# Kernel optimization log

Measured on AMD Instinct MI355X. Metric: run time of the kernel, lower is better.

Reference implementation:

```python
import jax, jax.numpy as jnp
import numpy as np

B, T, P, D = 8, 512, 2048, 768
TOKEN_HALF = 0.15
PATCH_HALF = 0.03  # small patch boxes


def _make_boxes(key, b, n, half):
    c = jax.random.uniform(key, (b, n, 2), dtype=jnp.float32)
    lo = jnp.clip(c - half, 0.0, 1.0)
    hi = jnp.clip(c + half, 0.0, 1.0)
    return jnp.concatenate([lo, hi], axis=-1)  # (b, n, 4): x0,y0,x1,y1


def setup_inputs() -> dict:
    key = jax.random.key(0)
    k1, k2, k3, k4 = jax.random.split(key, 4)
    patch_feats = jax.random.normal(k1, (B, P, D), dtype=jnp.float32)
    token_boxes = _make_boxes(k2, B, T, TOKEN_HALF)
    patch_boxes = _make_boxes(k3, B, P, PATCH_HALF)
    token_mask = jnp.ones((B, T), dtype=bool)
    scorer_w = jax.random.normal(k4, (D,), dtype=jnp.float32) * 0.02
    scorer_b = jnp.zeros((1,), dtype=jnp.float32)
    return {"patch_feats": patch_feats, "token_boxes": token_boxes,
            "patch_boxes": patch_boxes, "token_mask": token_mask,
            "scorer_w": scorer_w, "scorer_b": scorer_b}


def _patches_in_token_boxes(patch_boxes, tb):
    # patch center containment test: (B,T,P) bool
    cx = 0.5 * (patch_boxes[..., 0] + patch_boxes[..., 2])  # (B,P)
    cy = 0.5 * (patch_boxes[..., 1] + patch_boxes[..., 3])  # (B,P)
    cx = cx[:, None, :]
    cy = cy[:, None, :]
    return ((cx >= tb[..., 0:1]) & (cx <= tb[..., 2:3]) &
            (cy >= tb[..., 1:2]) & (cy <= tb[..., 3:4]))


def reference(patch_feats, token_boxes, patch_boxes, token_mask, scorer_w, scorer_b):
    # normalize token boxes if given in 0..1000 coords (data-dependent, via where)
    tb = token_boxes
    scale = jnp.where(tb.max() > 1.5, jnp.float32(1.0 / 1000.0), jnp.float32(1.0))
    tb = tb * scale

    in_box = _patches_in_token_boxes(patch_boxes, tb)          # (B,T,P)
    in_box = in_box & token_mask[:, :, None]
    region_mask = jnp.any(in_box, axis=-1)                      # (B,T)

    scores = patch_feats @ scorer_w + scorer_b[0]               # (B,P)
    scores = jnp.broadcast_to(scores[:, None, :], in_box.shape)  # (B,T,P)
    scores = jnp.where(in_box, scores, jnp.float32(-10000.0))
    attn = jax.nn.softmax(scores, axis=-1)                      # (B,T,P)

    region_feats = jnp.einsum('btp,bpd->btd', attn, patch_feats)
    region_feats = region_feats * region_mask[..., None].astype(region_feats.dtype)
    return region_feats, region_mask
```

## Files before the change

kernel.cpp:

```cpp
#include <hip/hip_runtime.h>

#define B 8
#define T 512
#define P 2048
#define D 768
#define KDIM P
#define NSPLIT 2
#define KSPLIT (KDIM / NSPLIT)

typedef unsigned short ushort_t;
using short8 = __attribute__((ext_vector_type(8))) short;
using f32x4v = __attribute__((ext_vector_type(4))) float;

#define IDX_SCALE 0
#define IDX_SCORES 64
#define IDX_SCORES2 (64 + B*P)
#define IDX_CX (64 + B*P)
#define IDX_CY (64 + 2*B*P)
#define OFF_ATTN_BYTES 197120
#define OFF_FT_BYTES (OFF_ATTN_BYTES + (size_t)B*T*P*2)
#define OFF_PART_BYTES (OFF_FT_BYTES + (size_t)B*D*P*2)
#define WS_NEED (OFF_PART_BYTES + (size_t)NSPLIT*B*T*D*4)

#define GLD16(gsrc, ldst) \
    __builtin_amdgcn_global_load_lds((const __attribute__((address_space(1))) void*)(gsrc), \
                                     (__attribute__((address_space(3))) void*)(ldst), 16, 0, 0)

#define SCHED_FENCE() __builtin_amdgcn_sched_barrier(0)
#define RAW_BARRIER() do { SCHED_FENCE(); __builtin_amdgcn_s_barrier(); SCHED_FENCE(); } while (0)

__device__ inline ushort_t f2bf(float x) {
    union { float f; unsigned u; } v; v.f = x;
    unsigned r = v.u + 0x7fffu + ((v.u >> 16) & 1u);
    return (ushort_t)(r >> 16);
}

__global__ void k_scale(const float* __restrict__ tboxes, float* __restrict__ ws) {
    __shared__ float red[4];
    int tid = threadIdx.x;
    float m = -1e30f;
    const float4* tb4 = (const float4*)tboxes;
    #pragma unroll
    for (int i = 0; i < 16; ++i) {
        float4 v = tb4[tid + i * 256];
        m = fmaxf(fmaxf(fmaxf(m, v.x), fmaxf(v.y, v.z)), v.w);
    }
    #pragma unroll
    for (int off = 1; off < 64; off <<= 1) m = fmaxf(m, __shfl_xor(m, off));
    if ((tid & 63) == 0) red[tid >> 6] = m;
    __syncthreads();
    if (tid == 0) {
        float mb = fmaxf(fmaxf(red[0], red[1]), fmaxf(red[2], red[3]));
        ws[IDX_SCALE] = (mb > 1.5f) ? (1.0f / 1000.0f) : 1.0f;
    }
}

__global__ __launch_bounds__(256) void k_prep(const float* __restrict__ feats,
        const float* __restrict__ w, float* __restrict__ ws, ushort_t* __restrict__ fT) {
    __shared__ float tile[2][64][65];
    __shared__ float sred[64][17];
    const int t = threadIdx.x;
    const int p0 = blockIdx.x * 64;
    const int z = blockIdx.y;
    const int b = blockIdx.z;
    const float4* f4 = (const float4*)(feats + ((size_t)b * P + p0) * D);
    const float4* w4 = (const float4*)w;
    const int tr = t >> 4, tc = t & 15;
    float sp[4] = {0.f, 0.f, 0.f, 0.f};

    float4 v[4];
    {
        int dt = z * 6;
        #pragma unroll
        for (int i = 0; i < 4; ++i)
            v[i] = f4[(size_t)(tr + 16 * i) * 192 + dt * 16 + tc];
    }
    int cur = 0;
    for (int it = 0; it < 6; ++it) {
        const int dt = z * 6 + it;
        float4 wv = w4[dt * 16 + tc];
        #pragma unroll
        for (int i = 0; i < 4; ++i) {
            int pr = tr + 16 * i;
            sp[i] += v[i].x * wv.x + v[i].y * wv.y + v[i].z * wv.z + v[i].w * wv.w;
            tile[cur][pr][tc * 4 + 0] = v[i].x;
            tile[cur][pr][tc * 4 + 1] = v[i].y;
            tile[cur][pr][tc * 4 + 2] = v[i].z;
            tile[cur][pr][tc * 4 + 3] = v[i].w;
        }
        __syncthreads();
        if (it < 5) {
            int dt2 = dt + 1;
            #pragma unroll
            for (int i = 0; i < 4; ++i)
                v[i] = f4[(size_t)(tr + 16 * i) * 192 + dt2 * 16 + tc];
        }
        #pragma unroll
        for (int pass = 0; pass < 4; ++pass) {
            int idx = pass * 256 + t;
            int dr = idx >> 4;
            int pq = (idx & 15) * 4;
            unsigned u0 = (unsigned)f2bf(tile[cur][pq + 0][dr]) |
                          ((unsigned)f2bf(tile[cur][pq + 1][dr]) << 16);
            unsigned u1 = (unsigned)f2bf(tile[cur][pq + 2][dr]) |
                          ((unsigned)f2bf(tile[cur][pq + 3][dr]) << 16);
            uint2 o; o.x = u0; o.y = u1;
            *(uint2*)&fT[((size_t)b * D + dt * 64 + dr) * P + p0 + pq] = o;
        }
        cur ^= 1;
    }
    #pragma unroll
    for (int i = 0; i < 4; ++i) sred[tr + 16 * i][tc] = sp[i];
    __syncthreads();
    if (t < 64) {
        float s = 0.f;
        #pragma unroll
        for (int c = 0; c < 16; ++c) s += sred[t][c];
        ws[(z ? IDX_SCORES2 : IDX_SCORES) + b * P + p0 + t] = s;
    }
}

__global__ __launch_bounds__(256) void k_attn(const float* __restrict__ tboxes,
        const float* __restrict__ pboxes, const unsigned char* __restrict__ mask8,
        const float* __restrict__ bias, const float* __restrict__ ws,
        ushort_t* __restrict__ attn, float* __restrict__ out) {
    const int wv = threadIdx.x >> 6;
    const int ln = threadIdx.x & 63;
    const int t = blockIdx.x * 4 + wv;
    const int b = blockIdx.y;
    const int row = b * T + t;
    const float scale = ws[IDX_SCALE];
    const float bs = bias[0];
    const float4 tb = ((const float4*)tboxes)[row];
    const float lox = tb.x * scale, loy = tb.y * scale;
    const float hix = tb.z * scale, hiy = tb.w * scale;
    bool storage_u8 = ((mask8[1] | mask8[2] | mask8[3]) != 0);
    bool tmask = storage_u8 ? (mask8[row] != 0) : (((const int*)mask8)[row] != 0);

    const float2* sA = (const float2*)(ws + IDX_SCORES + b * P);
    const float2* sB = (const float2*)(ws + IDX_SCORES2 + b * P);
    const float4* pb4 = (const float4*)(pboxes + (size_t)b * P * 4);
    unsigned* arow32 = (unsigned*)(attn + (size_t)row * P);

    float s0[16], s1[16];
    float m = -1e30f;
    const float NINF = -__builtin_inff();
    #pragma unroll
    for (int r = 0; r < 16; ++r) {
        int q = ln + 64 * r;
        float2 sa = sA[q], sb = sB[q];
        float v0 = sa.x + sb.x + bs;
        float v1 = sa.y + sb.y + bs;
        float4 b0 = pb4[2 * q], b1 = pb4[2 * q + 1];
        float cx0 = 0.5f * (b0.x + b0.z), cy0 = 0.5f * (b0.y + b0.w);
        float cx1 = 0.5f * (b1.x + b1.z), cy1 = 0.5f * (b1.y + b1.w);
        bool i0 = (cx0 >= lox) && (cx0 <= hix) && (cy0 >= loy) && (cy0 <= hiy);
        bool i1 = (cx1 >= lox) && (cx1 <= hix) && (cy1 >= loy) && (cy1 <= hiy);
        s0[r] = i0 ? v0 : NINF;
        s1[r] = i1 ? v1 : NINF;
        m = fmaxf(m, fmaxf(s0[r], s1[r]));
    }
    #pragma unroll
    for (int off = 1; off < 64; off <<= 1) m = fmaxf(m, __shfl_xor(m, off));
    bool any = m > -1e29f;

    if (!any || !tmask) {
        #pragma unroll
        for (int r = 0; r < 16; ++r) arow32[ln + 64 * r] = 0u;
        if (ln == 0) out[(size_t)B * T * D + row] = 0.f;
        return;
    }
    float lsum = 0.f;
    #pragma unroll
    for (int r = 0; r < 16; ++r) {
        s0[r] = __expf(s0[r] - m);
        s1[r] = __expf(s1[r] - m);
        lsum += s0[r] + s1[r];
    }
    #pragma unroll
    for (int off = 1; off < 64; off <<= 1) lsum += __shfl_xor(lsum, off);
    float invl = 1.0f / lsum;
    #pragma unroll
    for (int r = 0; r < 16; ++r) {
        unsigned lo = (unsigned)f2bf(s0[r] * invl);
        unsigned hi = (unsigned)f2bf(s1[r] * invl);
        arow32[ln + 64 * r] = lo | (hi << 16);
    }
    if (ln == 0) out[(size_t)B * T * D + row] = 1.0f;
}

__global__ __launch_bounds__(256, 2) void k_gemm(const ushort_t* __restrict__ attn,
        const ushort_t* __restrict__ fT, float* __restrict__ partial) {
    __shared__ __align__(16) ushort_t As[2 * 8192];
    __shared__ __align__(16) ushort_t Bs[2 * 8192];
    const int tid = threadIdx.x;
    const int lane = tid & 63, wid = tid >> 6;
    const int wm = wid >> 1, wn = wid & 1;

    const int bid = blockIdx.x;
    const int b = bid & 7;
    const int rem = bid >> 3;
    const int s = (rem >= 24) ? 1 : 0;
    const int tile = (rem >= 24) ? rem - 24 : rem;
    const int t0 = (tile & 3) * 128;
    const int n0 = (tile >> 2) * 128;
    const int kbase = s * KSPLIT;

    const ushort_t* Ab = attn + ((size_t)b * T + t0) * P + kbase;
    const ushort_t* Bb = fT + ((size_t)b * D + n0) * P + kbase;

    const int rl8 = lane >> 3;
    const int slot = (lane & 7) ^ rl8;

    f32x4v acc[4][4];
    #pragma unroll
    for (int i = 0; i < 4; ++i)
        #pragma unroll
        for (int j = 0; j < 4; ++j)
            acc[i][j] = (f32x4v){0.f, 0.f, 0.f, 0.f};

    const int lr = lane & 15, hi4 = lane >> 4;

    #define STAGE(buf, kt) do { \
        const ushort_t* a_src = Ab + (size_t)(kt) * 64; \
        const ushort_t* b_src = Bb + (size_t)(kt) * 64; \
        _Pragma("unroll") \
        for (int i = 0; i < 4; ++i) { \
            int c = wid * 4 + i; \
            GLD16(a_src + (size_t)(c * 8 + rl8) * P + slot * 8, &As[(buf) * 8192 + c * 512]); \
        } \
        _Pragma("unroll") \
        for (int i = 0; i < 4; ++i) { \
            int c = wid * 4 + i; \
            GLD16(b_src + (size_t)(c * 8 + rl8) * P + slot * 8, &Bs[(buf) * 8192 + c * 512]); \
        } \
    } while (0)

    #define LDA(row, kslot) (((row) >> 3) * 512 + ((row) & 7) * 64 + (((kslot) ^ ((row) & 7)) * 8))

    #define COMPUTE(buf) do { \
        _Pragma("unroll") \
        for (int ks = 0; ks < 2; ++ks) { \
            short8 a[4], bfr[4]; \
            int kslot = ks * 4 + hi4; \
            _Pragma("unroll") \
            for (int i = 0; i < 4; ++i) \
                a[i] = *(const short8*)&As[(buf) * 8192 + LDA(wm * 64 + i * 16 + lr, kslot)]; \
            _Pragma("unroll") \
            for (int j = 0; j < 4; ++j) \
                bfr[j] = *(const short8*)&Bs[(buf) * 8192 + LDA(wn * 64 + j * 16 + lr, kslot)]; \
            _Pragma("unroll") \
            for (int i = 0; i < 4; ++i) \
                _Pragma("unroll") \
                for (int j = 0; j < 4; ++j) \
                    acc[i][j] = __builtin_amdgcn_mfma_f32_16x16x32_bf16(a[i], bfr[j], acc[i][j], 0, 0, 0); \
        } \
    } while (0)

    STAGE(0, 0);
    int cur = 0;
    for (int kt = 0; kt < KSPLIT / 64 - 1; ++kt) {
        STAGE(cur ^ 1, kt + 1);
        asm volatile("s_waitcnt vmcnt(8)" ::: "memory");
        RAW_BARRIER();
        COMPUTE(cur);
        RAW_BARRIER();
        cur ^= 1;
    }
    asm volatile("s_waitcnt vmcnt(0)" ::: "memory");
    RAW_BARRIER();
    COMPUTE(cur);

    float* pout = partial + (size_t)s * B * T * D;
    #pragma unroll
    for (int i = 0; i < 4; ++i) {
        #pragma unroll
        for (int j = 0; j < 4; ++j) {
            int trow = t0 + wm * 64 + i * 16 + hi4 * 4;
            int ncol = n0 + wn * 64 + j * 16 + lr;
            #pragma unroll
            for (int q = 0; q < 4; ++q)
                pout[((size_t)(b * T) + trow + q) * D + ncol] = acc[i][j][q];
        }
    }
    #undef STAGE
    #undef LDA
    #undef COMPUTE
}

__global__ __launch_bounds__(256) void k_reduce(const float* __restrict__ partial,
                                                float* __restrict__ out) {
    const size_t i = (size_t)blockIdx.x * 256 + threadIdx.x;
    const size_t stride = (size_t)(B * T * D) / 4;
    const float4* p = (const float4*)partial;
    float4 a = p[i], b2 = p[i + stride];
    float4 r;
    r.x = a.x + b2.x;
    r.y = a.y + b2.y;
    r.z = a.z + b2.z;
    r.w = a.w + b2.w;
    ((float4*)out)[i] = r;
}

__global__ __launch_bounds__(256) void k_scores_fb(
        const float* __restrict__ feats, const float* __restrict__ pboxes,
        const float* __restrict__ w, const float* __restrict__ bias,
        float* __restrict__ ws) {
    int row = blockIdx.x * 4 + (threadIdx.x >> 6);
    int lane = threadIdx.x & 63;
    const float* f = feats + (size_t)row * D;
    float acc = 0.f;
    #pragma unroll
    for (int k = 0; k < D / 64; ++k) acc += f[lane + k * 64] * w[lane + k * 64];
    #pragma unroll
    for (int off = 1; off < 64; off <<= 1) acc += __shfl_xor(acc, off);
    if (lane == 0) {
        ws[IDX_SCORES + row] = acc + bias[0];
        ws[IDX_CX + row] = 0.5f * (pboxes[row * 4 + 0] + pboxes[row * 4 + 2]);
        ws[IDX_CY + row] = 0.5f * (pboxes[row * 4 + 1] + pboxes[row * 4 + 3]);
    }
}

__global__ __launch_bounds__(256) void k_main_fb(
        const float* __restrict__ feats, const float* __restrict__ tboxes,
        const unsigned char* __restrict__ mask8,
        const float* __restrict__ ws, float* __restrict__ out) {
    const int t = blockIdx.x, b = blockIdx.y;
    const int tid = threadIdx.x;
    const float scale = ws[IDX_SCALE];
    const float* scores = ws + IDX_SCORES;
    const float* cxs = ws + IDX_CX;
    const float* cys = ws + IDX_CY;
    const int row = b * T + t;
    const float lo_x = tboxes[row * 4 + 0] * scale;
    const float lo_y = tboxes[row * 4 + 1] * scale;
    const float hi_x = tboxes[row * 4 + 2] * scale;
    const float hi_y = tboxes[row * 4 + 3] * scale;
    bool storage_u8 = ((mask8[1] | mask8[2] | mask8[3]) != 0);
    bool tmask = storage_u8 ? (mask8[row] != 0) : (((const int*)mask8)[row] != 0);
    float s[8]; bool ib[8];
    float m = -1e30f;
    #pragma unroll
    for (int j = 0; j < 8; ++j) {
        int p = tid + j * 256;
        float cx = cxs[b * P + p], cy = cys[b * P + p];
        bool in = (cx >= lo_x) && (cx <= hi_x) && (cy >= lo_y) && (cy <= hi_y);
        ib[j] = in;
        s[j] = scores[b * P + p];
        if (in) m = fmaxf(m, s[j]);
    }
    __shared__ float s_red[4];
    #pragma unroll
    for (int off = 1; off < 64; off <<= 1) m = fmaxf(m, __shfl_xor(m, off));
    if ((tid & 63) == 0) s_red[tid >> 6] = m;
    __syncthreads();
    float mb = fmaxf(fmaxf(s_red[0], s_red[1]), fmaxf(s_red[2], s_red[3]));
    bool any = mb > -1e29f;
    const size_t obase = (size_t)row * D;
    if (!any || !tmask) {
        out[obase + tid] = 0.f; out[obase + tid + 256] = 0.f; out[obase + tid + 512] = 0.f;
        if (tid == 0) out[(size_t)B * T * D + row] = 0.f;
        return;
    }
    float w8[8]; int c = 0; float lsum = 0.f;
    #pragma unroll
    for (int j = 0; j < 8; ++j) {
        float wv = ib[j] ? __expf(s[j] - mb) : 0.f;
        w8[j] = wv; lsum += wv;
        if (ib[j]) ++c;
    }
    __shared__ float s_sum[4];
    #pragma unroll
    for (int off = 1; off < 64; off <<= 1) lsum += __shfl_xor(lsum, off);
    if ((tid & 63) == 0) s_sum[tid >> 6] = lsum;
    __syncthreads();
    float l = s_sum[0] + s_sum[1] + s_sum[2] + s_sum[3];
    __shared__ int s_cnt[256];
    s_cnt[tid] = c;
    __syncthreads();
    #pragma unroll
    for (int off = 1; off < 256; off <<= 1) {
        int v = (tid >= off) ? s_cnt[tid - off] : 0;
        __syncthreads();
        s_cnt[tid] += v;
        __syncthreads();
    }
    int excl = s_cnt[tid] - c;
    int nnz = s_cnt[255];
    __shared__ int s_idx[P];
    __shared__ float s_wt[P];
    int o = excl;
    #pragma unroll
    for (int j = 0; j < 8; ++j) {
        if (ib[j]) { s_idx[o] = tid + j * 256; s_wt[o] = w8[j]; ++o; }
    }
    __syncthreads();
    float a0 = 0.f, a1 = 0.f, a2 = 0.f;
    const float* fb = feats + (size_t)b * P * D;
    for (int i = 0; i < nnz; ++i) {
        int p = s_idx[i];
        float wv = s_wt[i];
        const float* fr = fb + (size_t)p * D + tid;
        a0 += wv * fr[0]; a1 += wv * fr[256]; a2 += wv * fr[512];
    }
    float inv = 1.0f / l;
    out[obase + tid] = a0 * inv;
    out[obase + tid + 256] = a1 * inv;
    out[obase + tid + 512] = a2 * inv;
    if (tid == 0) out[(size_t)B * T * D + row] = 1.0f;
}

extern "C" void kernel_launch(void* const* d_in, const int* in_sizes, int n_in,
                              void* d_out, int out_size, void* d_ws, size_t ws_size,
                              hipStream_t stream) {
    const float* feats  = (const float*)d_in[0];
    const float* tboxes = (const float*)d_in[1];
    const float* pboxes = (const float*)d_in[2];
    const unsigned char* tmask = (const unsigned char*)d_in[3];
    const float* w      = (const float*)d_in[4];
    const float* bias   = (const float*)d_in[5];
    float* out = (float*)d_out;
    float* ws  = (float*)d_ws;

    if (ws_size >= WS_NEED) {
        ushort_t* attn = (ushort_t*)((char*)d_ws + OFF_ATTN_BYTES);
        ushort_t* fT   = (ushort_t*)((char*)d_ws + OFF_FT_BYTES);
        float* part    = (float*)((char*)d_ws + OFF_PART_BYTES);
        k_scale<<<1, 256, 0, stream>>>(tboxes, ws);
        k_prep<<<dim3(P / 64, 2, B), 256, 0, stream>>>(feats, w, ws, fT);
        k_attn<<<dim3(T / 4, B), 256, 0, stream>>>(tboxes, pboxes, tmask, bias, ws, attn, out);
        k_gemm<<<dim3(NSPLIT * B * (T / 128) * (D / 128)), 256, 0, stream>>>(attn, fT, part);
        k_reduce<<<dim3(B * T * D / 4 / 256), 256, 0, stream>>>(part, out);
    } else {
        k_scale<<<1, 256, 0, stream>>>(tboxes, ws);
        k_scores_fb<<<(B * P) / 4, 256, 0, stream>>>(feats, pboxes, w, bias, ws);
        k_main_fb<<<dim3(T, B), 256, 0, stream>>>(feats, tboxes, tmask, ws, out);
    }
}
```

Measured before the change: 62.02 us.

## Store split-K partials in bf16 and remap GEMM block order

The GEMM now writes its split-K partial sums as bf16 instead of fp32, which halves the partial buffer and the traffic read by the reduce kernel. The reduce kernel unpacks bf16 pairs and handles eight outputs per thread. The block-index mapping is also reordered so that the two K-splits and four T-tiles of one batch and N-tile land on neighbouring block IDs, likely to improve L2 reuse of the fT tile. Rounding partial sums to bf16 costs accuracy in the final output.

```diff
diff --git a/kernel.cpp b/kernel.cpp
--- a/kernel.cpp
+++ b/kernel.cpp
@@ -20,7 +20,7 @@
 #define OFF_ATTN_BYTES 197120
 #define OFF_FT_BYTES (OFF_ATTN_BYTES + (size_t)B*T*P*2)
 #define OFF_PART_BYTES (OFF_FT_BYTES + (size_t)B*D*P*2)
-#define WS_NEED (OFF_PART_BYTES + (size_t)NSPLIT*B*T*D*4)
+#define WS_NEED (OFF_PART_BYTES + (size_t)NSPLIT*B*T*D*2)
 
 #define GLD16(gsrc, ldst) \
     __builtin_amdgcn_global_load_lds((const __attribute__((address_space(1))) void*)(gsrc), \
@@ -190,7 +190,7 @@
 }
 
 __global__ __launch_bounds__(256, 2) void k_gemm(const ushort_t* __restrict__ attn,
-        const ushort_t* __restrict__ fT, float* __restrict__ partial) {
+        const ushort_t* __restrict__ fT, ushort_t* __restrict__ partial) {
     __shared__ __align__(16) ushort_t As[2 * 8192];
     __shared__ __align__(16) ushort_t Bs[2 * 8192];
     const int tid = threadIdx.x;
@@ -198,12 +198,13 @@
     const int wm = wid >> 1, wn = wid & 1;
 
     const int bid = blockIdx.x;
-    const int b = bid & 7;
-    const int rem = bid >> 3;
-    const int s = (rem >= 24) ? 1 : 0;
-    const int tile = (rem >= 24) ? rem - 24 : rem;
-    const int t0 = (tile & 3) * 128;
-    const int n0 = (tile >> 2) * 128;
+    const int g = bid & 7;
+    const int i6 = bid >> 3;
+    const int tq = g & 3;
+    const int s = g >> 2;
+    const int b = i6 & 7;
+    const int n0 = (i6 >> 3) * 128;
+    const int t0 = tq * 128;
     const int kbase = s * KSPLIT;
 
     const ushort_t* Ab = attn + ((size_t)b * T + t0) * P + kbase;
@@ -271,7 +272,7 @@
     RAW_BARRIER();
     COMPUTE(cur);
 
-    float* pout = partial + (size_t)s * B * T * D;
+    ushort_t* pout = partial + (size_t)s * B * T * D;
     #pragma unroll
     for (int i = 0; i < 4; ++i) {
         #pragma unroll
@@ -280,7 +281,7 @@
             int ncol = n0 + wn * 64 + j * 16 + lr;
             #pragma unroll
             for (int q = 0; q < 4; ++q)
-                pout[((size_t)(b * T) + trow + q) * D + ncol] = acc[i][j][q];
+                pout[((size_t)(b * T) + trow + q) * D + ncol] = f2bf(acc[i][j][q]);
         }
     }
     #undef STAGE
@@ -288,18 +289,23 @@
     #undef COMPUTE
 }
 
-__global__ __launch_bounds__(256) void k_reduce(const float* __restrict__ partial,
+__global__ __launch_bounds__(256) void k_reduce(const ushort_t* __restrict__ partial,
                                                 float* __restrict__ out) {
     const size_t i = (size_t)blockIdx.x * 256 + threadIdx.x;
-    const size_t stride = (size_t)(B * T * D) / 4;
-    const float4* p = (const float4*)partial;
-    float4 a = p[i], b2 = p[i + stride];
-    float4 r;
-    r.x = a.x + b2.x;
-    r.y = a.y + b2.y;
-    r.z = a.z + b2.z;
-    r.w = a.w + b2.w;
-    ((float4*)out)[i] = r;
+    const size_t stride = (size_t)(B * T * D) / 8;
+    const uint4* p = (const uint4*)partial;
+    uint4 a = p[i], b2 = p[i + stride];
+    float4 r0, r1;
+    r0.x = __uint_as_float(a.x << 16)          + __uint_as_float(b2.x << 16);
+    r0.y = __uint_as_float(a.x & 0xffff0000u)  + __uint_as_float(b2.x & 0xffff0000u);
+    r0.z = __uint_as_float(a.y << 16)          + __uint_as_float(b2.y << 16);
+    r0.w = __uint_as_float(a.y & 0xffff0000u)  + __uint_as_float(b2.y & 0xffff0000u);
+    r1.x = __uint_as_float(a.z << 16)          + __uint_as_float(b2.z << 16);
+    r1.y = __uint_as_float(a.z & 0xffff0000u)  + __uint_as_float(b2.z & 0xffff0000u);
+    r1.z = __uint_as_float(a.w << 16)          + __uint_as_float(b2.w << 16);
+    r1.w = __uint_as_float(a.w & 0xffff0000u)  + __uint_as_float(b2.w & 0xffff0000u);
+    ((float4*)out)[2 * i]     = r0;
+    ((float4*)out)[2 * i + 1] = r1;
 }
 
 __global__ __launch_bounds__(256) void k_scores_fb(
@@ -425,12 +431,12 @@
     if (ws_size >= WS_NEED) {
         ushort_t* attn = (ushort_t*)((char*)d_ws + OFF_ATTN_BYTES);
         ushort_t* fT   = (ushort_t*)((char*)d_ws + OFF_FT_BYTES);
-        float* part    = (float*)((char*)d_ws + OFF_PART_BYTES);
+        ushort_t* part = (ushort_t*)((char*)d_ws + OFF_PART_BYTES);
         k_scale<<<1, 256, 0, stream>>>(tboxes, ws);
         k_prep<<<dim3(P / 64, 2, B), 256, 0, stream>>>(feats, w, ws, fT);
         k_attn<<<dim3(T / 4, B), 256, 0, stream>>>(tboxes, pboxes, tmask, bias, ws, attn, out);
         k_gemm<<<dim3(NSPLIT * B * (T / 128) * (D / 128)), 256, 0, stream>>>(attn, fT, part);
-        k_reduce<<<dim3(B * T * D / 4 / 256), 256, 0, stream>>>(part, out);
+        k_reduce<<<dim3(B * T * D / 8 / 256), 256, 0, stream>>>(part, out);
     } else {
         k_scale<<<1, 256, 0, stream>>>(tboxes, ws);
         k_scores_fb<<<(B * P) / 4, 256, 0, stream>>>(feats, pboxes, w, bias, ws);
```

Result: no change. 62.62 us (+1.0%).
